# Performance work log

Hardware: AMD Instinct MI355X
Metric: run time of the kernel (lower is better)

Reference implementation:

```python
import jax, jax.numpy as jnp
import numpy as np

N_HEADS = 16


def _rotate_half(x):
    x_even = x[..., ::2]
    x_odd = x[..., 1::2]
    return jnp.stack((-x_odd, x_even), axis=-1).reshape(x.shape)


def _apply_rope(x, cos, sin):
    # cos/sin: (S, d_head) broadcast against (B, H, S, d_head)
    return x * cos + _rotate_half(x) * sin


def setup_inputs() -> dict:
    key = jax.random.key(0)
    k1, k2, k3 = jax.random.split(key, 3)
    B, S, D, H = 2, 2048, 1024, N_HEADS
    dh = D // H
    x = jax.random.normal(k1, (B, S, D), dtype=jnp.float32)
    w_qkv = jax.random.normal(k2, (D, 3 * D), dtype=jnp.float32) * 0.02
    w_proj = jax.random.normal(k3, (D, D), dtype=jnp.float32) * 0.02
    # standard interleaved RoPE tables, shape (S, d_head)
    inv_freq = 1.0 / (10000.0 ** (jnp.arange(0, dh, 2, dtype=jnp.float32) / dh))
    angles = jnp.arange(S, dtype=jnp.float32)[:, None] * inv_freq[None, :]  # (S, dh/2)
    rope_cos = jnp.repeat(jnp.cos(angles), 2, axis=-1)  # (S, dh)
    rope_sin = jnp.repeat(jnp.sin(angles), 2, axis=-1)
    return {"x": x, "w_qkv": w_qkv, "w_proj": w_proj, "rope_cos": rope_cos, "rope_sin": rope_sin}


def reference(x, w_qkv, w_proj, rope_cos, rope_sin):
    B, S, D = x.shape
    H = N_HEADS
    dh = D // H
    half = dh // 2
    qkv = x @ w_qkv  # (B, S, 3D)
    q, k, v = jnp.split(qkv, 3, axis=-1)
    # (B, S, D) -> (B, H, S, dh)
    q = q.reshape(B, S, H, dh).transpose(0, 2, 1, 3)
    k = k.reshape(B, S, H, dh).transpose(0, 2, 1, 3)
    v = v.reshape(B, S, H, dh).transpose(0, 2, 1, 3)
    q = _apply_rope(q, rope_cos, rope_sin)
    k = _apply_rope(k, rope_cos, rope_sin)
    scale = half ** -0.5
    # dual score matrices from the two half-subspaces
    attn_up = jnp.einsum('bhid,bhjd->bhij', q[..., :half], k[..., :half]) * scale
    attn_down = jnp.einsum('bhid,bhjd->bhij', q[..., half:], k[..., half:]) * scale
    lower_mask = jnp.tril(jnp.ones((S, S), dtype=bool))  # j <= i -> down
    attn_logits = jnp.where(lower_mask, attn_down, attn_up)
    attn_weights = jax.nn.softmax(attn_logits, axis=-1)
    attn_out = jnp.einsum('bhij,bhjd->bhid', attn_weights, v)
    attn_out = attn_out.transpose(0, 2, 1, 3).reshape(B, S, D)
    return attn_out @ w_proj
```

## Files before the change

### kernel.cpp

```cpp
#include <hip/hip_runtime.h>
#include <hip/hip_bf16.h>
#include <stdint.h>

typedef __bf16 bf16;
typedef __attribute__((ext_vector_type(4))) __bf16 bf16x4;
typedef __attribute__((ext_vector_type(8))) __bf16 bf16x8;
typedef __attribute__((ext_vector_type(4))) float f32x4;

#define MFMA16(a, b, c) __builtin_amdgcn_mfma_f32_16x16x32_bf16((a), (b), (c), 0, 0, 0)

#define QSC (0.17677669529663687f * 1.4426950408889634f)

__device__ __forceinline__ void async_cp16(const bf16* g, bf16* l) {
  __builtin_amdgcn_global_load_lds(
      (const __attribute__((address_space(1))) void*)g,
      (__attribute__((address_space(3))) void*)l, 16, 0, 0);
}

__global__ __launch_bounds__(256) void convx_k(const float* __restrict__ in,
                                               bf16* __restrict__ out, int n) {
  int i = (blockIdx.x * 256 + threadIdx.x) * 4;
  const int stride = gridDim.x * 256 * 4;
  for (; i < n; i += stride) {
    const f32x4 f = *(const f32x4*)(in + i);
    bf16x4 o;
    o[0] = (bf16)f[0]; o[1] = (bf16)f[1]; o[2] = (bf16)f[2]; o[3] = (bf16)f[3];
    *(bf16x4*)(out + i) = o;
  }
}

__global__ __launch_bounds__(256) void transpose_k(const float* __restrict__ in,
                                                   bf16* __restrict__ out, int R, int C) {
  __shared__ bf16 t[64][65];
  const int bc = blockIdx.x * 64;
  const int br = blockIdx.y * 64;
  const int tx = threadIdx.x & 63, ty = threadIdx.x >> 6;
#pragma unroll
  for (int r = ty; r < 64; r += 4) t[r][tx] = (bf16)in[(br + r) * C + bc + tx];
  __syncthreads();
#pragma unroll
  for (int r = ty; r < 64; r += 4) out[(bc + r) * R + br + tx] = t[tx][r];
}

template <int MODE, int BM>
__global__ __launch_bounds__(256) void gemm128(
    const bf16* __restrict__ A, const bf16* __restrict__ BT, int M, int N, int K,
    float* __restrict__ C, bf16* __restrict__ qws, bf16* __restrict__ kws,
    bf16* __restrict__ vT, const float* __restrict__ ropeC, const float* __restrict__ ropeS) {
  constexpr int MT = BM / 32;
  __shared__ __align__(16) bf16 As[BM * 32];
  __shared__ __align__(16) bf16 Bs[128 * 32];
  const int tid = threadIdx.x;
  const int lane = tid & 63, wave = tid >> 6;
  const int l16 = lane & 15, quad = lane >> 4;
  const int wm = (wave >> 1) * (BM / 2), wn = (wave & 1) * 64;
  const int bm = blockIdx.y, bn = blockIdx.x;

  const bf16* ag = A + (bm * BM + (tid >> 2)) * K + (tid & 3) * 8;
  const bf16* bg = BT + (bn * 128 + (tid >> 2)) * K + (tid & 3) * 8;
  bf16* la = &As[tid * 8];
  bf16* lb = &Bs[tid * 8];

  f32x4 acc[MT][4] = {};

  for (int k0 = 0; k0 < K; k0 += 32) {
    async_cp16(ag + k0, la);
    if (BM == 128) async_cp16(ag + 64 * K + k0, la + 2048);
    async_cp16(bg + k0, lb);
    async_cp16(bg + 64 * K + k0, lb + 2048);
    __syncthreads();
    bf16x8 af[MT], bff[4];
#pragma unroll
    for (int t = 0; t < MT; ++t)
      af[t] = *(const bf16x8*)&As[(wm + t * 16 + l16) * 32 + quad * 8];
#pragma unroll
    for (int t = 0; t < 4; ++t)
      bff[t] = *(const bf16x8*)&Bs[(wn + t * 16 + l16) * 32 + quad * 8];
#pragma unroll
    for (int mt = 0; mt < MT; ++mt)
#pragma unroll
      for (int nt = 0; nt < 4; ++nt) acc[mt][nt] = MFMA16(af[mt], bff[nt], acc[mt][nt]);
    __syncthreads();
  }

  if (MODE == 0) {
#pragma unroll
    for (int mt = 0; mt < MT; ++mt)
#pragma unroll
      for (int i = 0; i < 4; ++i) {
        const int row = bm * BM + wm + mt * 16 + quad * 4 + i;
#pragma unroll
        for (int nt = 0; nt < 4; ++nt) {
          const int col = bn * 128 + wn + nt * 16 + l16;
          C[row * N + col] = acc[mt][nt][i];
        }
      }
  } else {
    bf16* tb = &Bs[wave * 512];
#pragma unroll
    for (int mt = 0; mt < MT; ++mt) {
      const int s0 = bm * BM + wm + mt * 16;
      const int b = s0 >> 11, sbase = s0 & 2047;
#pragma unroll
      for (int nt = 0; nt < 4; ++nt) {
        const int colb = bn * 128 + wn + nt * 16;
        const int sec = colb >> 10, rem = colb & 1023;
        const int h = rem >> 6, d0 = rem & 63;
        if (sec < 2) {
          const int d = d0 + l16;
#pragma unroll
          for (int i = 0; i < 4; ++i) {
            const int s = sbase + quad * 4 + i;
            float v = acc[mt][nt][i];
            float pr = __shfl_xor(v, 1);
            float rot = (d & 1) ? pr : -pr;
            float rv = v * ropeC[s * 64 + d] + rot * ropeS[s * 64 + d];
            if (sec == 0) rv *= QSC;
            tb[(quad * 4 + i) * 20 + l16] = (bf16)rv;
          }
          bf16* dst = ((sec == 0) ? qws : kws) + ((b * 16 + h) * 2048 + sbase) * 64 + d0;
          bf16x4 seg = *(const bf16x4*)&tb[l16 * 20 + quad * 4];
          *(bf16x4*)(dst + l16 * 64 + quad * 4) = seg;
        } else {
          const int d = d0 + l16;
          const int s4 = sbase + quad * 4;
          const int a = (s4 >> 4) & 3;
          const int p = (s4 & ~63) | ((a >> 1) * 32 + quad * 8 + (a & 1) * 4);
          bf16x4 pk;
#pragma unroll
          for (int i = 0; i < 4; ++i) pk[i] = (bf16)acc[mt][nt][i];
          *(bf16x4*)(vT + ((b * 16 + h) * 64 + d) * 2048 + p) = pk;
        }
      }
    }
  }
}

__global__ __launch_bounds__(256) void attn_k(const bf16* __restrict__ qws,
                                              const bf16* __restrict__ kws,
                                              const bf16* __restrict__ vT,
                                              bf16* __restrict__ aw) {
  __shared__ __align__(16) bf16 Ks[64 * 64];
  __shared__ __align__(16) bf16 Vs[64 * 64];
  const int tid = threadIdx.x;
  const int lane = tid & 63, wave = tid >> 6;
  const int l16 = lane & 15, quad = lane >> 4;
  const int bh = blockIdx.x >> 4, qblk = blockIdx.x & 15;
  const int b = bh >> 4, h = bh & 15;
  const int rbase = qblk * 128 + wave * 32;

  const bf16* qb = qws + (bh * 2048 + rbase) * 64;
  const bf16* kb = kws + bh * 2048 * 64;
  const bf16* vb = vT + bh * 64 * 2048;

  const int r0 = wave * 16 + (lane >> 3);
  const int c0 = ((lane & 7) - r0) & 7;
  const bf16* kst0 = kb + r0 * 64 + c0 * 8;
  const bf16* kst1 = kb + (r0 + 8) * 64 + c0 * 8;
  const bf16* vst0 = vb + r0 * 2048 + c0 * 8;
  const bf16* vst1 = vb + (r0 + 8) * 2048 + c0 * 8;
  bf16* kd0 = Ks + wave * 1024;
  bf16* kd1 = Ks + wave * 1024 + 512;
  bf16* vd0 = Vs + wave * 1024;
  bf16* vd1 = Vs + wave * 1024 + 512;

  bf16x8 qf[2][2];
#pragma unroll
  for (int g = 0; g < 2; ++g)
#pragma unroll
    for (int hf = 0; hf < 2; ++hf)
      qf[g][hf] = *(const bf16x8*)(qb + (g * 16 + l16) * 64 + hf * 32 + quad * 8);

  f32x4 o[2][4] = {};
  float lp[2] = {0.f, 0.f};
  const f32x4 zz = {};
  const int tdw = rbase >> 6;

#define ATTN_BODY(TM)                                                                 \
  {                                                                                   \
    _Pragma("unroll") for (int ks = 0; ks < 2; ++ks) {                                \
      bf16x8 vf[4];                                                                   \
      _Pragma("unroll") for (int ntd = 0; ntd < 4; ++ntd)                             \
        vf[ntd] = *(const bf16x8*)(Vs + (ntd * 16 + l16) * 64 +                       \
                                   ((ks * 4 + quad + l16) & 7) * 8);                  \
      bf16x8 kfU[2], kfD[2];                                                          \
      _Pragma("unroll") for (int s = 0; s < 2; ++s) {                                 \
        const int ro = ((ks * 2 + s) * 16 + l16) * 64;                                \
        if (TM != 0) kfU[s] = *(const bf16x8*)(Ks + ro + ((quad + l16) & 7) * 8);     \
        if (TM != 2) kfD[s] = *(const bf16x8*)(Ks + ro + ((4 + quad + l16) & 7) * 8); \
      }                                                                               \
      f32x4 sU[2][2], sD[2][2];                                                       \
      _Pragma("unroll") for (int s = 0; s < 2; ++s)                                   \
        _Pragma("unroll") for (int g = 0; g < 2; ++g) {                               \
          if (TM != 0) sU[s][g] = MFMA16(kfU[s], qf[g][0], zz);                       \
          if (TM != 2) sD[s][g] = MFMA16(kfD[s], qf[g][1], zz);                       \
        }                                                                             \
      _Pragma("unroll") for (int g = 0; g < 2; ++g) {                                 \
        bf16x8 af;                                                                    \
        float ls = 0.f;                                                               \
        _Pragma("unroll") for (int s = 0; s < 2; ++s)                                 \
          _Pragma("unroll") for (int r = 0; r < 4; ++r) {                             \
            float x;                                                                  \
            if (TM == 0) x = sD[s][g][r];                                             \
            else if (TM == 2) x = sU[s][g][r];                                        \
            else {                                                                    \
              const int jcol = jt * 64 + (ks * 2 + s) * 16 + quad * 4 + r;            \
              x = (jcol <= rbase + g * 16 + l16) ? sD[s][g][r] : sU[s][g][r];         \
            }                                                                         \
            float pe = exp2f(x);                                                      \
            ls += pe;                                                                 \
            af[s * 4 + r] = (bf16)pe;                                                 \
          }                                                                           \
        lp[g] += ls;                                                                  \
        _Pragma("unroll") for (int ntd = 0; ntd < 4; ++ntd)                           \
            o[g][ntd] = MFMA16(af, vf[ntd], o[g][ntd]);                               \
      }                                                                               \
    }                                                                                 \
  }

  for (int jt = 0; jt < 32; ++jt) {
    async_cp16(kst0 + jt * 4096, kd0);
    async_cp16(kst1 + jt * 4096, kd1);
    async_cp16(vst0 + jt * 64, vd0);
    async_cp16(vst1 + jt * 64, vd1);
    __syncthreads();
    if (jt < tdw) ATTN_BODY(0)
    else if (jt == tdw) ATTN_BODY(1)
    else ATTN_BODY(2)
    __syncthreads();
  }
#undef ATTN_BODY

#pragma unroll
  for (int g = 0; g < 2; ++g) {
    lp[g] += __shfl_xor(lp[g], 16);
    lp[g] += __shfl_xor(lp[g], 32);
  }
#pragma unroll
  for (int g = 0; g < 2; ++g) {
    float ir[4];
#pragma unroll
    for (int r = 0; r < 4; ++r) ir[r] = 1.0f / __shfl(lp[g], quad * 4 + r);
#pragma unroll
    for (int ntd = 0; ntd < 4; ++ntd)
#pragma unroll
      for (int r = 0; r < 4; ++r)
        aw[(b * 2048 + rbase + g * 16 + quad * 4 + r) * 1024 + h * 64 + ntd * 16 + l16] =
            (bf16)(o[g][ntd][r] * ir[r]);
  }
}

extern "C" void kernel_launch(void* const* d_in, const int* in_sizes, int n_in,
                              void* d_out, int out_size, void* d_ws, size_t ws_size,
                              hipStream_t stream) {
  const float* x = (const float*)d_in[0];
  const float* w_qkv = (const float*)d_in[1];
  const float* w_proj = (const float*)d_in[2];
  const float* ropeC = (const float*)d_in[3];
  const float* ropeS = (const float*)d_in[4];
  float* out = (float*)d_out;

  char* ws = (char*)d_ws;
  bf16* xb = (bf16*)ws;     ws += (size_t)4194304 * 2;
  bf16* wqkvT = (bf16*)ws;  ws += (size_t)3145728 * 2;
  bf16* wprojT = (bf16*)ws; ws += (size_t)1048576 * 2;
  bf16* qws = (bf16*)ws;    ws += (size_t)4194304 * 2;
  bf16* kws = (bf16*)ws;    ws += (size_t)4194304 * 2;
  bf16* vT = (bf16*)ws;     ws += (size_t)4194304 * 2;
  bf16* aw = (bf16*)ws;     ws += (size_t)4194304 * 2;

  convx_k<<<1024, 256, 0, stream>>>(x, xb, 4194304);
  transpose_k<<<dim3(3072 / 64, 1024 / 64), 256, 0, stream>>>(w_qkv, wqkvT, 1024, 3072);
  transpose_k<<<dim3(1024 / 64, 1024 / 64), 256, 0, stream>>>(w_proj, wprojT, 1024, 1024);

  gemm128<1, 128><<<dim3(3072 / 128, 4096 / 128), 256, 0, stream>>>(
      xb, wqkvT, 4096, 3072, 1024, nullptr, qws, kws, vT, ropeC, ropeS);
  attn_k<<<512, 256, 0, stream>>>(qws, kws, vT, aw);
  gemm128<0, 64><<<dim3(1024 / 128, 4096 / 64), 256, 0, stream>>>(
      aw, wprojT, 4096, 1024, 1024, out, nullptr, nullptr, nullptr, nullptr, nullptr);
}
```

Before: 217.1 us.

## Double-buffer K/V tiles in attention kernel to overlap loads with compute

Uses two LDS buffers for K and V tiles. Each iteration reads its current tile into registers first, then issues the async loads for the next tile, then runs the MFMA/softmax work, so global loads overlap with compute. This also drops one barrier per iteration. In exchange it doubles LDS use per block, which may reduce occupancy, and raises register pressure because the full tile's fragments are held in registers.

```diff
diff --git a/kernel.cpp b/kernel.cpp
--- a/kernel.cpp
+++ b/kernel.cpp
@@ -140,8 +140,8 @@
                                               const bf16* __restrict__ kws,
                                               const bf16* __restrict__ vT,
                                               bf16* __restrict__ aw) {
-  __shared__ __align__(16) bf16 Ks[64 * 64];
-  __shared__ __align__(16) bf16 Vs[64 * 64];
+  __shared__ __align__(16) bf16 Ks[2][64 * 64];
+  __shared__ __align__(16) bf16 Vs[2][64 * 64];
   const int tid = threadIdx.x;
   const int lane = tid & 63, wave = tid >> 6;
   const int l16 = lane & 15, quad = lane >> 4;
@@ -159,10 +159,16 @@
   const bf16* kst1 = kb + (r0 + 8) * 64 + c0 * 8;
   const bf16* vst0 = vb + r0 * 2048 + c0 * 8;
   const bf16* vst1 = vb + (r0 + 8) * 2048 + c0 * 8;
-  bf16* kd0 = Ks + wave * 1024;
-  bf16* kd1 = Ks + wave * 1024 + 512;
-  bf16* vd0 = Vs + wave * 1024;
-  bf16* vd1 = Vs + wave * 1024 + 512;
+
+#define STAGE(jtv)                                         \
+  {                                                        \
+    bf16* kdst = &Ks[(jtv) & 1][wave * 1024];              \
+    bf16* vdst = &Vs[(jtv) & 1][wave * 1024];              \
+    async_cp16(kst0 + (jtv) * 4096, kdst);                 \
+    async_cp16(kst1 + (jtv) * 4096, kdst + 512);           \
+    async_cp16(vst0 + (jtv) * 64, vdst);                   \
+    async_cp16(vst1 + (jtv) * 64, vdst + 512);             \
+  }
 
   bf16x8 qf[2][2];
 #pragma unroll
@@ -176,24 +182,30 @@
   const f32x4 zz = {};
   const int tdw = rbase >> 6;
 
-#define ATTN_BODY(TM)                                                                 \
+#define ATTN_BODY(TM, jt)                                                             \
   {                                                                                   \
-    _Pragma("unroll") for (int ks = 0; ks < 2; ++ks) {                                \
-      bf16x8 vf[4];                                                                   \
+    const bf16* Kb = Ks[(jt) & 1];                                                    \
+    const bf16* Vb = Vs[(jt) & 1];                                                    \
+    bf16x8 vf[2][4];                                                                  \
+    _Pragma("unroll") for (int ks = 0; ks < 2; ++ks)                                  \
       _Pragma("unroll") for (int ntd = 0; ntd < 4; ++ntd)                             \
-        vf[ntd] = *(const bf16x8*)(Vs + (ntd * 16 + l16) * 64 +                       \
-                                   ((ks * 4 + quad + l16) & 7) * 8);                  \
-      bf16x8 kfU[2], kfD[2];                                                          \
+        vf[ks][ntd] = *(const bf16x8*)(Vb + (ntd * 16 + l16) * 64 +                   \
+                                       ((ks * 4 + quad + l16) & 7) * 8);              \
+    bf16x8 kfU[2][2], kfD[2][2];                                                      \
+    _Pragma("unroll") for (int ks = 0; ks < 2; ++ks)                                  \
       _Pragma("unroll") for (int s = 0; s < 2; ++s) {                                 \
         const int ro = ((ks * 2 + s) * 16 + l16) * 64;                                \
-        if (TM != 0) kfU[s] = *(const bf16x8*)(Ks + ro + ((quad + l16) & 7) * 8);     \
-        if (TM != 2) kfD[s] = *(const bf16x8*)(Ks + ro + ((4 + quad + l16) & 7) * 8); \
+        if (TM != 0) kfU[ks][s] = *(const bf16x8*)(Kb + ro + ((quad + l16) & 7) * 8); \
+        if (TM != 2)                                                                  \
+          kfD[ks][s] = *(const bf16x8*)(Kb + ro + ((4 + quad + l16) & 7) * 8);        \
       }                                                                               \
+    if ((jt) + 1 < 32) STAGE((jt) + 1)                                                \
+    _Pragma("unroll") for (int ks = 0; ks < 2; ++ks) {                                \
       f32x4 sU[2][2], sD[2][2];                                                       \
       _Pragma("unroll") for (int s = 0; s < 2; ++s)                                   \
         _Pragma("unroll") for (int g = 0; g < 2; ++g) {                               \
-          if (TM != 0) sU[s][g] = MFMA16(kfU[s], qf[g][0], zz);                       \
-          if (TM != 2) sD[s][g] = MFMA16(kfD[s], qf[g][1], zz);                       \
+          if (TM != 0) sU[s][g] = MFMA16(kfU[ks][s], qf[g][0], zz);                   \
+          if (TM != 2) sD[s][g] = MFMA16(kfD[ks][s], qf[g][1], zz);                   \
         }                                                                             \
       _Pragma("unroll") for (int g = 0; g < 2; ++g) {                                 \
         bf16x8 af;                                                                    \
@@ -204,7 +216,7 @@
             if (TM == 0) x = sD[s][g][r];                                             \
             else if (TM == 2) x = sU[s][g][r];                                        \
             else {                                                                    \
-              const int jcol = jt * 64 + (ks * 2 + s) * 16 + quad * 4 + r;            \
+              const int jcol = (jt) * 64 + (ks * 2 + s) * 16 + quad * 4 + r;          \
               x = (jcol <= rbase + g * 16 + l16) ? sD[s][g][r] : sU[s][g][r];         \
             }                                                                         \
             float pe = exp2f(x);                                                      \
@@ -213,23 +225,21 @@
           }                                                                           \
         lp[g] += ls;                                                                  \
         _Pragma("unroll") for (int ntd = 0; ntd < 4; ++ntd)                           \
-            o[g][ntd] = MFMA16(af, vf[ntd], o[g][ntd]);                               \
+            o[g][ntd] = MFMA16(af, vf[ks][ntd], o[g][ntd]);                           \
       }                                                                               \
     }                                                                                 \
   }
 
+  STAGE(0)
   for (int jt = 0; jt < 32; ++jt) {
-    async_cp16(kst0 + jt * 4096, kd0);
-    async_cp16(kst1 + jt * 4096, kd1);
-    async_cp16(vst0 + jt * 64, vd0);
-    async_cp16(vst1 + jt * 64, vd1);
+    asm volatile("s_waitcnt vmcnt(0)" ::: "memory");
     __syncthreads();
-    if (jt < tdw) ATTN_BODY(0)
-    else if (jt == tdw) ATTN_BODY(1)
-    else ATTN_BODY(2)
-    __syncthreads();
+    if (jt < tdw) ATTN_BODY(0, jt)
+    else if (jt == tdw) ATTN_BODY(1, jt)
+    else ATTN_BODY(2, jt)
   }
 #undef ATTN_BODY
+#undef STAGE
 
 #pragma unroll
   for (int g = 0; g < 2; ++g) {
```

New measurement: 216.1 us. About the same (-0.5%).
